# Optimization experiments

Measured on AMD Instinct MI355X. Metric: run time of the kernel, lower is better.

The kernel has to match this reference:

```python
import jax, jax.numpy as jnp
import numpy as np

B = 16
DRUG_LEN, PROT_LEN = 64, 1200
DIM, CONV = 64, 40


def conv1d(x, w, b):
    # x: [B, C_in, L], w: [C_out, C_in, K] (torch layout), VALID padding
    y = jax.lax.conv_general_dilated(
        x, w, window_strides=(1,), padding='VALID',
        dimension_numbers=('NCH', 'OIH', 'NCH'))
    return y + b[None, :, None]


def setup_inputs() -> dict:
    key = jax.random.key(0)
    ks = jax.random.split(key, 32)
    s = 0.05
    inp = {
        'drug_tokens': jax.random.randint(ks[0], (B, DRUG_LEN), 0, 65, dtype=jnp.int32),
        'protein_tokens': jax.random.randint(ks[1], (B, PROT_LEN), 0, 26, dtype=jnp.int32),
        'drug_emb': (jax.random.normal(ks[2], (65, DIM)) * s).at[0].set(0.0),
        'prot_emb': (jax.random.normal(ks[3], (26, DIM)) * s).at[0].set(0.0),
        'dW1': jax.random.normal(ks[4], (CONV, DIM, 4)) * s,
        'db1': jax.random.normal(ks[5], (CONV,)) * s,
        'dW2': jax.random.normal(ks[6], (CONV * 2, CONV, 6)) * s,
        'db2': jax.random.normal(ks[7], (CONV * 2,)) * s,
        'dW3': jax.random.normal(ks[8], (CONV * 4, CONV * 2, 8)) * s,
        'db3': jax.random.normal(ks[9], (CONV * 4,)) * s,
        'pW1': jax.random.normal(ks[10], (CONV, DIM, 4)) * s,
        'pb1': jax.random.normal(ks[11], (CONV,)) * s,
        'pW2': jax.random.normal(ks[12], (CONV * 2, CONV, 8)) * s,
        'pb2': jax.random.normal(ks[13], (CONV * 2,)) * s,
        'pW3': jax.random.normal(ks[14], (CONV * 4, CONV * 2, 12)) * s,
        'pb3': jax.random.normal(ks[15], (CONV * 4,)) * s,
        'dattW': jax.random.normal(ks[16], (160, 160)) * s,
        'dattb': jax.random.normal(ks[17], (160,)) * s,
        'pattW': jax.random.normal(ks[18], (160, 160)) * s,
        'pattb': jax.random.normal(ks[19], (160,)) * s,
        'attW': jax.random.normal(ks[20], (160, 160)) * s,
        'attb': jax.random.normal(ks[21], (160,)) * s,
        'fc1W': jax.random.normal(ks[22], (1024, 320)) * s,
        'fc1b': jax.random.normal(ks[23], (1024,)) * s,
        'fc2W': jax.random.normal(ks[24], (1024, 1024)) * s,
        'fc2b': jax.random.normal(ks[25], (1024,)) * s,
        'fc3W': jax.random.normal(ks[26], (512, 1024)) * s,
        'fc3b': jax.random.normal(ks[27], (512,)) * s,
        'outW': jax.random.normal(ks[28], (2, 512)) * s,
        'outb': jax.random.normal(ks[29], (2,)) * s,
    }
    return inp


def reference(drug_tokens, protein_tokens, drug_emb, prot_emb,
              dW1, db1, dW2, db2, dW3, db3,
              pW1, pb1, pW2, pb2, pW3, pb3,
              dattW, dattb, pattW, pattb, attW, attb,
              fc1W, fc1b, fc2W, fc2b, fc3W, fc3b, outW, outb):
    relu = jax.nn.relu
    # Embedding lookup, then to [B, C, L]
    de = drug_emb[drug_tokens].transpose(0, 2, 1)    # [B,64,64]
    pe = prot_emb[protein_tokens].transpose(0, 2, 1)  # [B,64,1200]
    # CNN stacks
    dc = relu(conv1d(relu(conv1d(relu(conv1d(de, dW1, db1)), dW2, db2)), dW3, db3))  # [B,160,49]
    pc = relu(conv1d(relu(conv1d(relu(conv1d(pe, pW1, pb1)), pW2, pb2)), pW3, pb3))  # [B,160,1179]
    # Per-token attention projections (Linear over channel dim)
    d_att = jnp.einsum('bcd,oc->bdo', dc, dattW) + dattb   # [B,49,160]
    p_att = jnp.einsum('bcp,oc->bpo', pc, pattW) + pattb   # [B,1179,160]
    # Broadcast outer-sum + ReLU + Linear  -> [B,49,1179,160]
    A = relu(d_att[:, :, None, :] + p_att[:, None, :, :])
    A = jnp.einsum('bdpk,ok->bdpo', A, attW) + attb
    comp_atte = jax.nn.sigmoid(jnp.mean(A, axis=2)).transpose(0, 2, 1)  # [B,160,49]
    prot_atte = jax.nn.sigmoid(jnp.mean(A, axis=1)).transpose(0, 2, 1)  # [B,160,1179]
    dc = dc * 0.5 + dc * comp_atte
    pc = pc * 0.5 + pc * prot_atte
    # Global max pool over length
    dvec = jnp.max(dc, axis=2)  # [B,160]
    pvec = jnp.max(pc, axis=2)  # [B,160]
    pair = jnp.concatenate([dvec, pvec], axis=1)  # [B,320]
    # MLP head (dropout = identity at inference)
    h = jax.nn.leaky_relu(pair @ fc1W.T + fc1b, 0.01)
    h = jax.nn.leaky_relu(h @ fc2W.T + fc2b, 0.01)
    h = jax.nn.leaky_relu(h @ fc3W.T + fc3b, 0.01)
    return h @ outW.T + outb  # [B,2]
```

## Files before the change

kernel.cpp:

```cpp
#include <hip/hip_runtime.h>
#include <hip/hip_bf16.h>

typedef __hip_bfloat16 bf16;
typedef __attribute__((ext_vector_type(8))) short short8;
typedef __attribute__((ext_vector_type(4))) float floatx4;

#define NB 16


__device__ __forceinline__ float b2f(bf16 x) { return __bfloat162float(x); }
__device__ __forceinline__ float u16bf(unsigned short u) {
    return __uint_as_float(((unsigned)u) << 16);
}
__device__ __forceinline__ unsigned short f2bu(float v) {
    union { bf16 h; unsigned short u; } cv;
    cv.h = __float2bfloat16(v);
    return cv.u;
}

__global__ void sniff_kernel(const unsigned short* __restrict__ w, int* __restrict__ flag) {
    __shared__ int cnt;
    if (threadIdx.x == 0) cnt = 0;
    __syncthreads();
    int hits = 0;
    for (int s = 0; s < 4; s++) {
        unsigned short u = w[(threadIdx.x * 4 + s) * 2];
        float v = fabsf(u16bf(u));
        if (v > 1e-6f && v < 2.0f) hits++;
    }
    atomicAdd(&cnt, hits);
    __syncthreads();
    if (threadIdx.x == 0) *flag = (cnt > 512) ? 1 : 0;
}

#define NSEG 14
struct CvtJob {
    const void* src[NSEG];
    float* dst[NSEG];
    int n[NSEG];
};
#define NPK 11
struct PackJob {
    const void* src[NPK];
    bf16* dst[NPK];
    short Cout[NPK], CIN[NPK], K[NPK], coP[NPK], CIP[NPK];
};

__global__ void prep(CvtJob cj, PackJob pj, const int* __restrict__ flagp) {
    int y = blockIdx.y;
    int i = blockIdx.x * 256 + threadIdx.x;
    if (y < NSEG) {
        if (i >= cj.n[y]) return;
        const void* s = cj.src[y];
        if (s == nullptr) { cj.dst[y][i] = 0.f; return; }
        cj.dst[y][i] = (*flagp) ? b2f(((const bf16*)s)[i]) : ((const float*)s)[i];
    } else {
        int p = y - NSEG;
        int Cout = pj.Cout[p], CIN = pj.CIN[p], K = pj.K[p];
        int coP = pj.coP[p], CIP = pj.CIP[p];
        int total = K * coP * CIP;
        if (i >= total) return;
        int ci = i % CIP;
        int t = i / CIP;
        int co = t % coP;
        int k = t / coP;
        float v = 0.f;
        if (co < Cout && ci < CIN) {
            int s = (co * CIN + ci) * K + k;
            v = (*flagp) ? b2f(((const bf16*)pj.src[p])[s]) : ((const float*)pj.src[p])[s];
        }
        pj.dst[p][i] = __float2bfloat16(v);
    }
}

template <int K, int CIN, int CHUNKS, int NW>
__device__ __forceinline__ void conv_body(unsigned short* xT,
                                          const unsigned short* xb,
                                          const unsigned short* wbase,
                                          const float* __restrict__ bias,
                                          bf16* __restrict__ y,
                                          int b, int Lin, int Lout,
                                          int Cout, int coP, int l0) {
    const int CIP = CHUNKS * 32;
    const int PCI = CIP + 8;
    const int TLX = 64 + K - 1;
    for (int i = threadIdx.x; i < TLX * CIP; i += NW * 64) {
        int ci = i / TLX, l = i - ci * TLX;
        unsigned short v = 0;
        int gl = l0 + l;
        if (ci < CIN && gl < Lin) v = xb[ci * Lin + gl];
        xT[l * PCI + ci] = v;
    }
    __syncthreads();
    int lane = threadIdx.x & 63;
    int ct = threadIdx.x >> 6;
    int n = lane & 15, quad = lane >> 4;
    floatx4 acc[4];
#pragma unroll
    for (int i = 0; i < 4; i++) acc[i] = (floatx4){0.f, 0.f, 0.f, 0.f};
#pragma unroll
    for (int k = 0; k < K; k++) {
#pragma unroll
        for (int ch = 0; ch < CHUNKS; ch++) {
            short8 a = *(const short8*)(wbase +
                        ((size_t)(k * coP + ct * 16 + n)) * CIP + ch * 32 + quad * 8);
#pragma unroll
            for (int nt = 0; nt < 4; nt++) {
                short8 bb = *(const short8*)(xT + (nt * 16 + n + k) * PCI + ch * 32 + quad * 8);
                acc[nt] = __builtin_amdgcn_mfma_f32_16x16x32_bf16(a, bb, acc[nt], 0, 0, 0);
            }
        }
    }
    int m0 = quad * 4;
#pragma unroll
    for (int nt = 0; nt < 4; nt++) {
        int l = l0 + nt * 16 + n;
        if (l >= Lout) continue;
#pragma unroll
        for (int r = 0; r < 4; r++) {
            int co = ct * 16 + m0 + r;
            if (co < Cout)
                y[((size_t)b * Cout + co) * Lout + l] =
                    __float2bfloat16(fmaxf(acc[nt][r] + bias[co], 0.f));
        }
    }
}

template <int KD, int KP, int CIN, int CHUNKS, int NW>
__global__ __launch_bounds__(NW * 64) void conv_dual(const bf16* __restrict__ xd,
                                                 const bf16* __restrict__ Wpd,
                                                 const float* __restrict__ bd,
                                                 bf16* __restrict__ yd, int LinD, int LoutD,
                                                 const bf16* __restrict__ xp,
                                                 const bf16* __restrict__ Wpp,
                                                 const float* __restrict__ bp,
                                                 bf16* __restrict__ yp, int LinP, int LoutP,
                                                 int Cout, int coP) {
    const int CIP = CHUNKS * 32;
    const int PCI = CIP + 8;
    const int TLXMAX = 64 + KP - 1;
    __shared__ __align__(16) unsigned short xT[TLXMAX * PCI];
    if (blockIdx.x < 16) {
        int b = blockIdx.x;
        conv_body<KD, CIN, CHUNKS, NW>(xT, (const unsigned short*)xd + (size_t)b * CIN * LinD,
                                   (const unsigned short*)Wpd, bd, yd, b, LinD, LoutD,
                                   Cout, coP, 0);
    } else {
        int bx = blockIdx.x - 16;
        int b = bx / 19, l0 = (bx % 19) << 6;
        conv_body<KP, CIN, CHUNKS, NW>(xT, (const unsigned short*)xp + (size_t)b * CIN * LinP,
                                   (const unsigned short*)Wpp, bp, yp, b, LinP, LoutP,
                                   Cout, coP, l0);
    }
}

template <int K, int CIN, int CHUNKS, int NW>
__device__ __forceinline__ void conv_proj_phase(unsigned short* xT, unsigned short* xP,
                                                const unsigned short* xb,
                                                const unsigned short* wbase,
                                                const float* __restrict__ bias,
                                                unsigned short* __restrict__ y,
                                                int b, int Lin, int Lout,
                                                int Cout, int coP, int l0) {
    const int CIP = CHUNKS * 32;
    const int PCI = CIP + 8;
    const int TLX = 64 + K - 1;
    for (int i = threadIdx.x; i < TLX * CIP; i += NW * 64) {
        int ci = i / TLX, l = i - ci * TLX;
        unsigned short v = 0;
        int gl = l0 + l;
        if (ci < CIN && gl < Lin) v = xb[ci * Lin + gl];
        xT[l * PCI + ci] = v;
    }
    __syncthreads();
    int lane = threadIdx.x & 63;
    int ct = threadIdx.x >> 6;
    int n = lane & 15, quad = lane >> 4;
    floatx4 acc[4];
#pragma unroll
    for (int i = 0; i < 4; i++) acc[i] = (floatx4){0.f, 0.f, 0.f, 0.f};
#pragma unroll
    for (int k = 0; k < K; k++) {
#pragma unroll
        for (int ch = 0; ch < CHUNKS; ch++) {
            short8 a = *(const short8*)(wbase +
                        ((size_t)(k * coP + ct * 16 + n)) * CIP + ch * 32 + quad * 8);
#pragma unroll
            for (int nt = 0; nt < 4; nt++) {
                short8 bb = *(const short8*)(xT + (nt * 16 + n + k) * PCI + ch * 32 + quad * 8);
                acc[nt] = __builtin_amdgcn_mfma_f32_16x16x32_bf16(a, bb, acc[nt], 0, 0, 0);
            }
        }
    }
    int m0 = quad * 4;
#pragma unroll
    for (int nt = 0; nt < 4; nt++) {
        int ll = nt * 16 + n;
        int l = l0 + ll;
#pragma unroll
        for (int r = 0; r < 4; r++) {
            int co = ct * 16 + m0 + r;
            float val = (l < Lout) ? fmaxf(acc[nt][r] + bias[co], 0.f) : 0.f;
            unsigned short u = f2bu(val);
            xP[ll * 168 + co] = u;
            if (l < Lout) y[((size_t)b * Cout + co) * Lout + l] = u;
        }
    }
}

template <int KD, int KP, int CIN, int CHUNKS, int NW>
__global__ __launch_bounds__(NW * 64) void conv3_proj(
        const bf16* __restrict__ xd, const bf16* __restrict__ Wpd,
        const float* __restrict__ bd, bf16* __restrict__ yd, int LinD, int LoutD,
        const bf16* __restrict__ xp, const bf16* __restrict__ Wpp,
        const float* __restrict__ bp, bf16* __restrict__ yp, int LinP, int LoutP,
        int Cout, int coP,
        const bf16* __restrict__ dWB, const bf16* __restrict__ pWB,
        const float* __restrict__ dbF, const float* __restrict__ pbF,
        float* __restrict__ datt, bf16* __restrict__ pattB) {
    const int CIP = CHUNKS * 32;
    const int PCI = CIP + 8;
    const int TLXMAX = 64 + KP - 1;
    __shared__ __align__(16) unsigned short xT[TLXMAX * PCI];
    __shared__ __align__(16) unsigned short xP[64 * 168];
    bool isD = blockIdx.x < 16;
    int b, l0, L;
    if (isD) {
        b = blockIdx.x; l0 = 0; L = LoutD;
        conv_proj_phase<KD, CIN, CHUNKS, NW>(xT, xP,
            (const unsigned short*)xd + (size_t)b * CIN * LinD,
            (const unsigned short*)Wpd, bd, (unsigned short*)yd, b, LinD, LoutD, Cout, coP, 0);
    } else {
        int bx = blockIdx.x - 16;
        b = bx / 19; l0 = (bx % 19) << 6; L = LoutP;
        conv_proj_phase<KP, CIN, CHUNKS, NW>(xT, xP,
            (const unsigned short*)xp + (size_t)b * CIN * LinP,
            (const unsigned short*)Wpp, bp, (unsigned short*)yp, b, LinP, LoutP, Cout, coP, l0);
    }
    __syncthreads();
    int lane = threadIdx.x & 63;
    int t = threadIdx.x >> 6;
    int n = lane & 15, quad = lane >> 4;
    const unsigned short* W = (const unsigned short*)(isD ? dWB : pWB);
    const float* pbias = isD ? dbF : pbF;
    floatx4 acc[4];
#pragma unroll
    for (int i = 0; i < 4; i++) acc[i] = (floatx4){0.f, 0.f, 0.f, 0.f};
#pragma unroll
    for (int ch = 0; ch < 5; ch++) {
        short8 a = *(const short8*)(W + ((size_t)(t * 16 + n)) * 160 + ch * 32 + quad * 8);
#pragma unroll
        for (int nt = 0; nt < 4; nt++) {
            short8 bb = *(const short8*)(xP + (nt * 16 + n) * 168 + ch * 32 + quad * 8);
            acc[nt] = __builtin_amdgcn_mfma_f32_16x16x32_bf16(a, bb, acc[nt], 0, 0, 0);
        }
    }
    int m0 = quad * 4;
    int o0 = t * 16 + m0;
#pragma unroll
    for (int nt = 0; nt < 4; nt++) {
        int l = l0 + nt * 16 + n;
        if (l >= L) continue;
        if (isD) {
            float4 v;
            v.x = acc[nt][0] + pbias[o0 + 0];
            v.y = acc[nt][1] + pbias[o0 + 1];
            v.z = acc[nt][2] + pbias[o0 + 2];
            v.w = acc[nt][3] + pbias[o0 + 3];
            *(float4*)(datt + ((size_t)b * 49 + l) * 160 + o0) = v;
        } else {
            ushort4 u;
            u.x = f2bu(acc[nt][0] + pbias[o0 + 0]);
            u.y = f2bu(acc[nt][1] + pbias[o0 + 1]);
            u.z = f2bu(acc[nt][2] + pbias[o0 + 2]);
            u.w = f2bu(acc[nt][3] + pbias[o0 + 3]);
            *(ushort4*)((unsigned short*)pattB + ((size_t)b * 1179 + l) * 160 + o0) = u;
        }
    }
}

__global__ __launch_bounds__(256) void conv1_mfma(const int* __restrict__ dtok,
                                                  const int* __restrict__ ptok,
                                                  const bf16* __restrict__ embDB,
                                                  const bf16* __restrict__ embPB,
                                                  const bf16* __restrict__ dW1p,
                                                  const bf16* __restrict__ pW1p,
                                                  const float* __restrict__ db1f,
                                                  const float* __restrict__ pb1f,
                                                  bf16* __restrict__ d1,
                                                  bf16* __restrict__ p1) {
    const int K = 4, CIP = 64, PCI = 72, TLX = 67, coP = 48, Cout = 40;
    __shared__ __align__(16) unsigned short xT[TLX * PCI];
    __shared__ int stok[TLX];
    bool isD = blockIdx.x < 16;
    int b, l0, Lin, Lout;
    const int* tok; const unsigned short* embB; const unsigned short* Wp;
    const float* bias; bf16* y;
    if (isD) {
        b = blockIdx.x; l0 = 0; Lin = 64; Lout = 61;
        tok = dtok; embB = (const unsigned short*)embDB;
        Wp = (const unsigned short*)dW1p; bias = db1f; y = d1;
    } else {
        int bx = blockIdx.x - 16;
        b = bx / 19; l0 = (bx % 19) << 6; Lin = 1200; Lout = 1197;
        tok = ptok; embB = (const unsigned short*)embPB;
        Wp = (const unsigned short*)pW1p; bias = pb1f; y = p1;
    }
    if (threadIdx.x < TLX) {
        int l = l0 + threadIdx.x;
        stok[threadIdx.x] = (l < Lin) ? tok[b * Lin + l] : -1;
    }
    __syncthreads();
    for (int i = threadIdx.x; i < TLX * CIP; i += 256) {
        int ci = i / TLX, l = i - ci * TLX;
        int t = stok[l];
        xT[l * PCI + ci] = (t >= 0) ? embB[t * 64 + ci] : (unsigned short)0;
    }
    __syncthreads();
    int lane = threadIdx.x & 63;
    int w = threadIdx.x >> 6;
    int n = lane & 15, quad = lane >> 4;
    if (w >= 3) return;
    floatx4 acc[4];
#pragma unroll
    for (int i = 0; i < 4; i++) acc[i] = (floatx4){0.f, 0.f, 0.f, 0.f};
#pragma unroll
    for (int k = 0; k < K; k++) {
#pragma unroll
        for (int ch = 0; ch < 2; ch++) {
            short8 a = *(const short8*)(Wp +
                        ((size_t)(k * coP + w * 16 + n)) * CIP + ch * 32 + quad * 8);
#pragma unroll
            for (int nt = 0; nt < 4; nt++) {
                short8 bb = *(const short8*)(xT + (nt * 16 + n + k) * PCI + ch * 32 + quad * 8);
                acc[nt] = __builtin_amdgcn_mfma_f32_16x16x32_bf16(a, bb, acc[nt], 0, 0, 0);
            }
        }
    }
    int m0 = quad * 4;
#pragma unroll
    for (int nt = 0; nt < 4; nt++) {
        int l = l0 + nt * 16 + n;
        if (l >= Lout) continue;
#pragma unroll
        for (int r = 0; r < 4; r++) {
            int co = w * 16 + m0 + r;
            if (co < Cout)
                y[((size_t)b * Cout + co) * Lout + l] =
                    __float2bfloat16(fmaxf(acc[nt][r] + bias[co], 0.f));
        }
    }
}

__global__ __launch_bounds__(640) void mean_fused(const float* __restrict__ datt,
                                                  const bf16* __restrict__ patt,
                                                  bf16* __restrict__ MpW,
                                                  float* __restrict__ Mdpart) {
    __shared__ __align__(16) unsigned short sp[37 * 160];
    int tid = threadIdx.x;
    int b = blockIdx.x >> 5;
    int pc = blockIdx.x & 31;
    int p0 = pc * 37;
    int pmax = 1179 - p0;
    if (pmax > 37) pmax = 37;
    {
        const short8* src = (const short8*)((const unsigned short*)patt +
                                            ((size_t)b * 1179 + p0) * 160);
        short8* dst = (short8*)sp;
        int n8 = (pmax * 160) >> 3;
        for (int v = tid; v < n8; v += 640) dst[v] = src[v];
    }
    int h = tid & 3;
    int k = tid >> 2;
    int d0 = h * 13;
    int nd = (h == 3) ? 10 : 13;
    const float* drow = datt + (size_t)b * 49 * 160 + k;
    float dv[13], md[13];
#pragma unroll
    for (int i = 0; i < 13; i++) {
        dv[i] = (i < nd) ? drow[(d0 + i) * 160] : -1e30f;
        md[i] = 0.f;
    }
    __syncthreads();
    unsigned short* mp = (unsigned short*)MpW + ((size_t)b * 1184 + p0) * 160 + k;
#pragma unroll 2
    for (int pi = 0; pi < pmax; pi++) {
        float pv = u16bf(sp[pi * 160 + k]);
        float s0 = 0.f, s1 = 0.f, s2 = 0.f, s3 = 0.f;
#pragma unroll
        for (int g = 0; g < 3; g++) {
            float r0 = fmaxf(dv[g * 4 + 0] + pv, 0.f);
            float r1 = fmaxf(dv[g * 4 + 1] + pv, 0.f);
            float r2 = fmaxf(dv[g * 4 + 2] + pv, 0.f);
            float r3 = fmaxf(dv[g * 4 + 3] + pv, 0.f);
            md[g * 4 + 0] += r0; s0 += r0;
            md[g * 4 + 1] += r1; s1 += r1;
            md[g * 4 + 2] += r2; s2 += r2;
            md[g * 4 + 3] += r3; s3 += r3;
        }
        {
            float r = fmaxf(dv[12] + pv, 0.f);
            md[12] += r; s0 += r;
        }
        float s = (s0 + s1) + (s2 + s3);
        s += __shfl_xor(s, 1, 64);
        s += __shfl_xor(s, 2, 64);
        if (h == 0) mp[(size_t)pi * 160] = f2bu(s * (1.f / 49.f));
    }
    float* op = Mdpart + (((size_t)b * 32 + pc) * 49) * 160 + k;
#pragma unroll
    for (int i = 0; i < 13; i++)
        if (i < nd) op[(d0 + i) * 160] = md[i];
}

__global__ __launch_bounds__(640) void att_sig_mfma(const float* __restrict__ Mdpart,
                                                    const bf16* __restrict__ MpW,
                                                    const bf16* __restrict__ wattB,
                                                    const float* __restrict__ attbF,
                                                    const bf16* __restrict__ dcB,
                                                    const bf16* __restrict__ pcB,
                                                    float* __restrict__ pair) {
    const int PCI = 168;
    __shared__ __align__(16) unsigned short sM[64 * PCI];
    bool isD = blockIdx.x < 16;
    int b, p0, L, off;
    const unsigned short* conv;
    if (isD) {
        b = blockIdx.x; p0 = 0; L = 49; off = 0; conv = (const unsigned short*)dcB;
        const float* mdp = Mdpart + (size_t)b * 32 * 49 * 160;
        for (int i = threadIdx.x; i < 160 * 64; i += 640) {
            int r = i / 160, k = i - r * 160;
            float v = 0.f;
            if (r < 49) {
                const float* src = mdp + r * 160 + k;
                float s0 = 0.f, s1 = 0.f, s2 = 0.f, s3 = 0.f;
#pragma unroll
                for (int pc = 0; pc < 32; pc += 4) {
                    s0 += src[(size_t)(pc + 0) * 7840];
                    s1 += src[(size_t)(pc + 1) * 7840];
                    s2 += src[(size_t)(pc + 2) * 7840];
                    s3 += src[(size_t)(pc + 3) * 7840];
                }
                v = ((s0 + s1) + (s2 + s3)) * (1.f / 1179.f);
            }
            sM[r * PCI + k] = f2bu(v);
        }
    } else {
        int bx = blockIdx.x - 16;
        b = bx / 19; p0 = (bx % 19) << 6; L = 1179; off = 160;
        conv = (const unsigned short*)pcB;
        const unsigned short* mb = (const unsigned short*)MpW + (size_t)b * 1184 * 160;
        for (int i = threadIdx.x; i < 160 * 64; i += 640) {
            int r = i / 160, k = i - r * 160;
            int p = p0 + r;
            sM[r * PCI + k] = (p < 1179) ? mb[(size_t)p * 160 + k] : (unsigned short)0;
        }
    }
    __syncthreads();
    int lane = threadIdx.x & 63;
    int t = threadIdx.x >> 6;
    int n = lane & 15, quad = lane >> 4;
    floatx4 acc[4];
#pragma unroll
    for (int i = 0; i < 4; i++) acc[i] = (floatx4){0.f, 0.f, 0.f, 0.f};
    const unsigned short* W = (const unsigned short*)wattB;
#pragma unroll
    for (int ch = 0; ch < 5; ch++) {
        short8 a = *(const short8*)(W + ((size_t)(t * 16 + n)) * 160 + ch * 32 + quad * 8);
#pragma unroll
        for (int nt = 0; nt < 4; nt++) {
            short8 bb = *(const short8*)(sM + (nt * 16 + n) * PCI + ch * 32 + quad * 8);
            acc[nt] = __builtin_amdgcn_mfma_f32_16x16x32_bf16(a, bb, acc[nt], 0, 0, 0);
        }
    }
    int m0 = quad * 4;
    float vmax[4] = {0.f, 0.f, 0.f, 0.f};
#pragma unroll
    for (int nt = 0; nt < 4; nt++) {
        int p = p0 + nt * 16 + n;
#pragma unroll
        for (int r = 0; r < 4; r++) {
            int o = t * 16 + m0 + r;
            float sig = 1.f / (1.f + __expf(-(acc[nt][r] + attbF[o])));
            float v = 0.f;
            if (p < L) v = u16bf(conv[((size_t)b * 160 + o) * L + p]) * (0.5f + sig);
            vmax[r] = fmaxf(vmax[r], v);
        }
    }
#pragma unroll
    for (int m = 1; m < 16; m <<= 1) {
#pragma unroll
        for (int r = 0; r < 4; r++)
            vmax[r] = fmaxf(vmax[r], __shfl_xor(vmax[r], m, 64));
    }
    if (n == 0) {
#pragma unroll
        for (int r = 0; r < 4; r++)
            atomicMax((unsigned int*)(pair + b * 320 + off + t * 16 + m0 + r),
                      __float_as_uint(vmax[r]));
    }
}

__global__ __launch_bounds__(256) void fc_block(const float* __restrict__ in,
                                                const void* __restrict__ W,
                                                const float* __restrict__ bias,
                                                float* __restrict__ out,
                                                int IN, int OUT,
                                                const int* __restrict__ flagp) {
    int j = blockIdx.x;
    int w = threadIdx.x >> 6, li = threadIdx.x & 63;
    int nv = IN >> 2;
    const float4* i0 = (const float4*)(in + (size_t)(w * 4 + 0) * IN);
    const float4* i1 = (const float4*)(in + (size_t)(w * 4 + 1) * IN);
    const float4* i2 = (const float4*)(in + (size_t)(w * 4 + 2) * IN);
    const float4* i3 = (const float4*)(in + (size_t)(w * 4 + 3) * IN);
    float p0 = 0.f, p1 = 0.f, p2 = 0.f, p3 = 0.f;
    if (*flagp) {
        const ushort4* w4 = (const ushort4*)((const unsigned short*)W + (size_t)j * IN);
        for (int v = li; v < nv; v += 64) {
            ushort4 u = w4[v];
            float wa = u16bf(u.x), wb = u16bf(u.y), wc = u16bf(u.z), wd = u16bf(u.w);
            float4 x;
            x = i0[v]; p0 += x.x * wa + x.y * wb + x.z * wc + x.w * wd;
            x = i1[v]; p1 += x.x * wa + x.y * wb + x.z * wc + x.w * wd;
            x = i2[v]; p2 += x.x * wa + x.y * wb + x.z * wc + x.w * wd;
            x = i3[v]; p3 += x.x * wa + x.y * wb + x.z * wc + x.w * wd;
        }
    } else {
        const float4* w4 = (const float4*)((const float*)W + (size_t)j * IN);
        for (int v = li; v < nv; v += 64) {
            float4 u = w4[v];
            float4 x;
            x = i0[v]; p0 += x.x * u.x + x.y * u.y + x.z * u.z + x.w * u.w;
            x = i1[v]; p1 += x.x * u.x + x.y * u.y + x.z * u.z + x.w * u.w;
            x = i2[v]; p2 += x.x * u.x + x.y * u.y + x.z * u.z + x.w * u.w;
            x = i3[v]; p3 += x.x * u.x + x.y * u.y + x.z * u.z + x.w * u.w;
        }
    }
#pragma unroll
    for (int m = 1; m < 64; m <<= 1) {
        p0 += __shfl_xor(p0, m, 64);
        p1 += __shfl_xor(p1, m, 64);
        p2 += __shfl_xor(p2, m, 64);
        p3 += __shfl_xor(p3, m, 64);
    }
    if (li == 0) {
        float bj = bias[j];
        float o0 = p0 + bj, o1 = p1 + bj, o2 = p2 + bj, o3 = p3 + bj;
        o0 = o0 > 0.f ? o0 : 0.01f * o0;
        o1 = o1 > 0.f ? o1 : 0.01f * o1;
        o2 = o2 > 0.f ? o2 : 0.01f * o2;
        o3 = o3 > 0.f ? o3 : 0.01f * o3;
        out[(size_t)(w * 4 + 0) * OUT + j] = o0;
        out[(size_t)(w * 4 + 1) * OUT + j] = o1;
        out[(size_t)(w * 4 + 2) * OUT + j] = o2;
        out[(size_t)(w * 4 + 3) * OUT + j] = o3;
    }
}

__global__ __launch_bounds__(256) void out_block(const float* __restrict__ h,
                                                 const void* __restrict__ W,
                                                 const float* __restrict__ biasF,
                                                 void* __restrict__ out,
                                                 const int* __restrict__ flagp) {
    int j = blockIdx.x;
    int w = threadIdx.x >> 6, li = threadIdx.x & 63;
    const int IN = 512, nv = 128;
    const float4* i0 = (const float4*)(h + (size_t)(w * 4 + 0) * IN);
    const float4* i1 = (const float4*)(h + (size_t)(w * 4 + 1) * IN);
    const float4* i2 = (const float4*)(h + (size_t)(w * 4 + 2) * IN);
    const float4* i3 = (const float4*)(h + (size_t)(w * 4 + 3) * IN);
    float p0 = 0.f, p1 = 0.f, p2 = 0.f, p3 = 0.f;
    int flag = *flagp;
    if (flag) {
        const ushort4* w4 = (const ushort4*)((const unsigned short*)W + (size_t)j * IN);
        for (int v = li; v < nv; v += 64) {
            ushort4 u = w4[v];
            float wa = u16bf(u.x), wb = u16bf(u.y), wc = u16bf(u.z), wd = u16bf(u.w);
            float4 x;
            x = i0[v]; p0 += x.x * wa + x.y * wb + x.z * wc + x.w * wd;
            x = i1[v]; p1 += x.x * wa + x.y * wb + x.z * wc + x.w * wd;
            x = i2[v]; p2 += x.x * wa + x.y * wb + x.z * wc + x.w * wd;
            x = i3[v]; p3 += x.x * wa + x.y * wb + x.z * wc + x.w * wd;
        }
    } else {
        const float4* w4 = (const float4*)((const float*)W + (size_t)j * IN);
        for (int v = li; v < nv; v += 64) {
            float4 u = w4[v];
            float4 x;
            x = i0[v]; p0 += x.x * u.x + x.y * u.y + x.z * u.z + x.w * u.w;
            x = i1[v]; p1 += x.x * u.x + x.y * u.y + x.z * u.z + x.w * u.w;
            x = i2[v]; p2 += x.x * u.x + x.y * u.y + x.z * u.z + x.w * u.w;
            x = i3[v]; p3 += x.x * u.x + x.y * u.y + x.z * u.z + x.w * u.w;
        }
    }
#pragma unroll
    for (int m = 1; m < 64; m <<= 1) {
        p0 += __shfl_xor(p0, m, 64);
        p1 += __shfl_xor(p1, m, 64);
        p2 += __shfl_xor(p2, m, 64);
        p3 += __shfl_xor(p3, m, 64);
    }
    if (li == 0) {
        float bj = biasF[j];
        float o0 = p0 + bj, o1 = p1 + bj, o2 = p2 + bj, o3 = p3 + bj;
        if (flag) {
            bf16* ob = (bf16*)out;
            ob[(w * 4 + 0) * 2 + j] = __float2bfloat16(o0);
            ob[(w * 4 + 1) * 2 + j] = __float2bfloat16(o1);
            ob[(w * 4 + 2) * 2 + j] = __float2bfloat16(o2);
            ob[(w * 4 + 3) * 2 + j] = __float2bfloat16(o3);
        } else {
            float* of = (float*)out;
            of[(w * 4 + 0) * 2 + j] = o0;
            of[(w * 4 + 1) * 2 + j] = o1;
            of[(w * 4 + 2) * 2 + j] = o2;
            of[(w * 4 + 3) * 2 + j] = o3;
        }
    }
}

extern "C" void kernel_launch(void* const* d_in, const int* in_sizes, int n_in,
                              void* d_out, int out_size, void* d_ws, size_t ws_size,
                              hipStream_t stream) {
    const int* drug_tok = (const int*)d_in[0];
    const int* prot_tok = (const int*)d_in[1];
    const void* drug_emb = d_in[2];
    const void* prot_emb = d_in[3];
    const void* dW1 = d_in[4];  const void* db1 = d_in[5];
    const void* dW2 = d_in[6];  const void* db2 = d_in[7];
    const void* dW3 = d_in[8];  const void* db3 = d_in[9];
    const void* pW1 = d_in[10]; const void* pb1 = d_in[11];
    const void* pW2 = d_in[12]; const void* pb2 = d_in[13];
    const void* pW3 = d_in[14]; const void* pb3 = d_in[15];
    const void* dattW = d_in[16]; const void* dattb = d_in[17];
    const void* pattW = d_in[18]; const void* pattb = d_in[19];
    const void* attW  = d_in[20]; const void* attb  = d_in[21];
    const void* fc1W = d_in[22]; const void* fc1b = d_in[23];
    const void* fc2W = d_in[24]; const void* fc2b = d_in[25];
    const void* fc3W = d_in[26]; const void* fc3b = d_in[27];
    const void* outW = d_in[28]; const void* outb = d_in[29];

    char* base = (char*)d_ws;
    size_t cur = 0;
    auto alloc = [&](size_t bytes) -> char* {
        char* p = base + cur;
        cur = (cur + bytes + 255) & ~(size_t)255;
        return p;
    };
    int*   flag  = (int*)alloc(256);
    bf16* embDB = (bf16*)alloc(65 * 64 * 2);
    bf16* embPB = (bf16*)alloc(26 * 64 * 2);
    bf16* dW1p = (bf16*)alloc((size_t)4 * 48 * 64 * 2);
    bf16* pW1p = (bf16*)alloc((size_t)4 * 48 * 64 * 2);
    bf16* dW2p = (bf16*)alloc((size_t)6 * 128 * 64 * 2);
    bf16* dW3p = (bf16*)alloc((size_t)8 * 192 * 96 * 2);
    bf16* pW2p = (bf16*)alloc((size_t)8 * 128 * 64 * 2);
    bf16* pW3p = (bf16*)alloc((size_t)12 * 192 * 96 * 2);
    float* db1f = (float*)alloc(40 * 4);
    float* db2f = (float*)alloc(80 * 4);
    float* db3f = (float*)alloc(160 * 4);
    float* pb1f = (float*)alloc(40 * 4);
    float* pb2f = (float*)alloc(80 * 4);
    float* pb3f = (float*)alloc(160 * 4);
    float* dattbF = (float*)alloc(160 * 4);
    float* pattbF = (float*)alloc(160 * 4);
    float* attbF  = (float*)alloc(160 * 4);
    float* fc1bF = (float*)alloc(1024 * 4);
    float* fc2bF = (float*)alloc(1024 * 4);
    float* fc3bF = (float*)alloc(512 * 4);
    float* outbF = (float*)alloc(2 * 4);
    bf16* dattWB = (bf16*)alloc(25600 * 2);
    bf16* pattWB = (bf16*)alloc(25600 * 2);
    bf16* wattB  = (bf16*)alloc(25600 * 2);
    bf16* d1  = (bf16*)alloc((size_t)NB * 40 * 61 * 2);
    bf16* d2  = (bf16*)alloc((size_t)NB * 80 * 56 * 2);
    bf16* dcB = (bf16*)alloc((size_t)NB * 160 * 49 * 2);
    bf16* p1  = (bf16*)alloc((size_t)NB * 40 * 1197 * 2);
    bf16* p2  = (bf16*)alloc((size_t)NB * 80 * 1190 * 2);
    bf16* pcB = (bf16*)alloc((size_t)NB * 160 * 1179 * 2);
    float* datt  = (float*)alloc((size_t)NB * 49 * 160 * 4);
    bf16* pattB = (bf16*)alloc((size_t)NB * 1179 * 160 * 2);
    float* Mdpart = (float*)alloc((size_t)NB * 32 * 49 * 160 * 4);
    bf16* MpW  = (bf16*)alloc((size_t)NB * 1184 * 160 * 2);
    float* pair = (float*)alloc(NB * 320 * 4);
    float* h1 = (float*)alloc(NB * 1024 * 4);
    float* h2 = (float*)alloc(NB * 1024 * 4);
    float* h3 = (float*)alloc(NB * 512 * 4);

    sniff_kernel<<<1, 256, 0, stream>>>((const unsigned short*)fc2W, flag);

    CvtJob cj;
    int si = 0;
    auto add = [&](const void* s, float* d, int n) { cj.src[si] = s; cj.dst[si] = d; cj.n[si] = n; si++; };
    add(db1, db1f, 40); add(db2, db2f, 80); add(db3, db3f, 160);
    add(pb1, pb1f, 40); add(pb2, pb2f, 80); add(pb3, pb3f, 160);
    add(dattb, dattbF, 160); add(pattb, pattbF, 160); add(attb, attbF, 160);
    add(fc1b, fc1bF, 1024); add(fc2b, fc2bF, 1024); add(fc3b, fc3bF, 512);
    add(outb, outbF, 2);
    add(nullptr, pair, NB * 320);
    PackJob pj;
    int pi = 0;
    auto seg = [&](const void* s, bf16* d, int Cout, int CIN, int K, int coP, int CIP) {
        pj.src[pi] = s; pj.dst[pi] = d;
        pj.Cout[pi] = Cout; pj.CIN[pi] = CIN; pj.K[pi] = K; pj.coP[pi] = coP; pj.CIP[pi] = CIP;
        pi++;
    };
    seg(dW1, dW1p, 40, 64, 4, 48, 64);
    seg(pW1, pW1p, 40, 64, 4, 48, 64);
    seg(dW2, dW2p, 80, 40, 6, 128, 64);
    seg(pW2, pW2p, 80, 40, 8, 128, 64);
    seg(dW3, dW3p, 160, 80, 8, 192, 96);
    seg(pW3, pW3p, 160, 80, 12, 192, 96);
    seg(dattW, dattWB, 160, 160, 1, 160, 160);
    seg(pattW, pattWB, 160, 160, 1, 160, 160);
    seg(attW,  wattB,  160, 160, 1, 160, 160);
    seg(drug_emb, embDB, 65, 64, 1, 65, 64);
    seg(prot_emb, embPB, 26, 64, 1, 26, 64);
    prep<<<dim3(864, NSEG + NPK), 256, 0, stream>>>(cj, pj, flag);

    conv1_mfma<<<16 + 16 * 19, 256, 0, stream>>>(drug_tok, prot_tok, embDB, embPB,
                                                 dW1p, pW1p, db1f, pb1f, d1, p1);
    conv_dual<6, 8, 40, 2, 5><<<320, 320, 0, stream>>>(
        d1, dW2p, db2f, d2, 61, 56,
        p1, pW2p, pb2f, p2, 1197, 1190, 80, 128);
    conv3_proj<8, 12, 80, 3, 10><<<320, 640, 0, stream>>>(
        d2, dW3p, db3f, dcB, 56, 49,
        p2, pW3p, pb3f, pcB, 1190, 1179, 160, 192,
        dattWB, pattWB, dattbF, pattbF, datt, pattB);

    mean_fused<<<16 * 32, 640, 0, stream>>>(datt, pattB, MpW, Mdpart);

    att_sig_mfma<<<320, 640, 0, stream>>>(Mdpart, MpW, wattB, attbF, dcB, pcB, pair);

    fc_block<<<1024, 256, 0, stream>>>(pair, fc1W, fc1bF, h1, 320, 1024, flag);
    fc_block<<<1024, 256, 0, stream>>>(h1, fc2W, fc2bF, h2, 1024, 1024, flag);
    fc_block<<<512, 256, 0, stream>>>(h2, fc3W, fc3bF, h3, 1024, 512, flag);
    out_block<<<2, 256, 0, stream>>>(h3, outW, outbF, d_out, flag);
}
```

Measured before the change: 241.8 us.

## Vectorize conv input staging, pad conv1 output stride, flatten prep launch grid

```diff
diff --git a/kernel.cpp b/kernel.cpp
--- a/kernel.cpp
+++ b/kernel.cpp
@@ -37,7 +37,6 @@
 struct CvtJob {
     const void* src[NSEG];
     float* dst[NSEG];
-    int n[NSEG];
 };
 #define NPK 11
 struct PackJob {
@@ -45,29 +44,33 @@
     bf16* dst[NPK];
     short Cout[NPK], CIN[NPK], K[NPK], coP[NPK], CIP[NPK];
 };
-
-__global__ void prep(CvtJob cj, PackJob pj, const int* __restrict__ flagp) {
-    int y = blockIdx.y;
-    int i = blockIdx.x * 256 + threadIdx.x;
-    if (y < NSEG) {
-        if (i >= cj.n[y]) return;
-        const void* s = cj.src[y];
-        if (s == nullptr) { cj.dst[y][i] = 0.f; return; }
-        cj.dst[y][i] = (*flagp) ? b2f(((const bf16*)s)[i]) : ((const float*)s)[i];
+struct PrepOff { int off[NSEG + NPK + 1]; };
+
+__global__ void prep(CvtJob cj, PackJob pj, PrepOff po, const int* __restrict__ flagp) {
+    int g = blockIdx.x * 256 + threadIdx.x;
+    if (g >= po.off[NSEG + NPK]) return;
+    int s = 0;
+#pragma unroll
+    for (int t = 1; t < NSEG + NPK; t++)
+        if (g >= po.off[t]) s = t;
+    int i = g - po.off[s];
+    if (s < NSEG) {
+        const void* sp = cj.src[s];
+        if (sp == nullptr) { cj.dst[s][i] = 0.f; return; }
+        cj.dst[s][i] = (*flagp) ? b2f(((const bf16*)sp)[i]) : ((const float*)sp)[i];
     } else {
-        int p = y - NSEG;
+        int p = s - NSEG;
         int Cout = pj.Cout[p], CIN = pj.CIN[p], K = pj.K[p];
         int coP = pj.coP[p], CIP = pj.CIP[p];
-        int total = K * coP * CIP;
-        if (i >= total) return;
+        (void)K;
         int ci = i % CIP;
         int t = i / CIP;
         int co = t % coP;
         int k = t / coP;
         float v = 0.f;
         if (co < Cout && ci < CIN) {
-            int s = (co * CIN + ci) * K + k;
-            v = (*flagp) ? b2f(((const bf16*)pj.src[p])[s]) : ((const float*)pj.src[p])[s];
+            int si = (co * CIN + ci) * pj.K[p] + k;
+            v = (*flagp) ? b2f(((const bf16*)pj.src[p])[si]) : ((const float*)pj.src[p])[si];
         }
         pj.dst[p][i] = __float2bfloat16(v);
     }
@@ -79,17 +82,27 @@
                                           const unsigned short* wbase,
                                           const float* __restrict__ bias,
                                           bf16* __restrict__ y,
-                                          int b, int Lin, int Lout,
+                                          int b, int Lin, int Lstride, int Lout,
                                           int Cout, int coP, int l0) {
     const int CIP = CHUNKS * 32;
     const int PCI = CIP + 8;
     const int TLX = 64 + K - 1;
-    for (int i = threadIdx.x; i < TLX * CIP; i += NW * 64) {
-        int ci = i / TLX, l = i - ci * TLX;
-        unsigned short v = 0;
-        int gl = l0 + l;
-        if (ci < CIN && gl < Lin) v = xb[ci * Lin + gl];
-        xT[l * PCI + ci] = v;
+    const int LV = (TLX + 7) >> 3;
+    for (int i = threadIdx.x; i < CIP * LV; i += NW * 64) {
+        int ci = i / LV, lv = (i - ci * LV) << 3;
+        if (ci < CIN && lv + 8 <= TLX && l0 + lv + 8 <= Lin) {
+            short8 v = *(const short8*)(xb + ci * Lstride + l0 + lv);
+#pragma unroll
+            for (int j = 0; j < 8; j++) xT[(lv + j) * PCI + ci] = (unsigned short)v[j];
+        } else {
+            for (int j = 0; j < 8; j++) {
+                int l = lv + j;
+                if (l >= TLX) break;
+                int gl = l0 + l;
+                xT[l * PCI + ci] = (ci < CIN && gl < Lin) ? xb[ci * Lstride + gl]
+                                                          : (unsigned short)0;
+            }
+        }
     }
     __syncthreads();
     int lane = threadIdx.x & 63;
@@ -130,11 +143,13 @@
 __global__ __launch_bounds__(NW * 64) void conv_dual(const bf16* __restrict__ xd,
                                                  const bf16* __restrict__ Wpd,
                                                  const float* __restrict__ bd,
-                                                 bf16* __restrict__ yd, int LinD, int LoutD,
+                                                 bf16* __restrict__ yd,
+                                                 int LinD, int LsD, int LoutD,
                                                  const bf16* __restrict__ xp,
                                                  const bf16* __restrict__ Wpp,
                                                  const float* __restrict__ bp,
-                                                 bf16* __restrict__ yp, int LinP, int LoutP,
+                                                 bf16* __restrict__ yp,
+                                                 int LinP, int LsP, int LoutP,
                                                  int Cout, int coP) {
     const int CIP = CHUNKS * 32;
     const int PCI = CIP + 8;
@@ -142,14 +157,14 @@
     __shared__ __align__(16) unsigned short xT[TLXMAX * PCI];
     if (blockIdx.x < 16) {
         int b = blockIdx.x;
-        conv_body<KD, CIN, CHUNKS, NW>(xT, (const unsigned short*)xd + (size_t)b * CIN * LinD,
-                                   (const unsigned short*)Wpd, bd, yd, b, LinD, LoutD,
+        conv_body<KD, CIN, CHUNKS, NW>(xT, (const unsigned short*)xd + (size_t)b * CIN * LsD,
+                                   (const unsigned short*)Wpd, bd, yd, b, LinD, LsD, LoutD,
                                    Cout, coP, 0);
     } else {
         int bx = blockIdx.x - 16;
         int b = bx / 19, l0 = (bx % 19) << 6;
-        conv_body<KP, CIN, CHUNKS, NW>(xT, (const unsigned short*)xp + (size_t)b * CIN * LinP,
-                                   (const unsigned short*)Wpp, bp, yp, b, LinP, LoutP,
+        conv_body<KP, CIN, CHUNKS, NW>(xT, (const unsigned short*)xp + (size_t)b * CIN * LsP,
+                                   (const unsigned short*)Wpp, bp, yp, b, LinP, LsP, LoutP,
                                    Cout, coP, l0);
     }
 }
@@ -165,12 +180,22 @@
     const int CIP = CHUNKS * 32;
     const int PCI = CIP + 8;
     const int TLX = 64 + K - 1;
-    for (int i = threadIdx.x; i < TLX * CIP; i += NW * 64) {
-        int ci = i / TLX, l = i - ci * TLX;
-        unsigned short v = 0;
-        int gl = l0 + l;
-        if (ci < CIN && gl < Lin) v = xb[ci * Lin + gl];
-        xT[l * PCI + ci] = v;
+    const int LV = (TLX + 7) >> 3;
+    for (int i = threadIdx.x; i < CIP * LV; i += NW * 64) {
+        int ci = i / LV, lv = (i - ci * LV) << 3;
+        if (ci < CIN && lv + 8 <= TLX && l0 + lv + 8 <= Lin) {
+            short8 v = *(const short8*)(xb + ci * Lin + l0 + lv);
+#pragma unroll
+            for (int j = 0; j < 8; j++) xT[(lv + j) * PCI + ci] = (unsigned short)v[j];
+        } else {
+            for (int j = 0; j < 8; j++) {
+                int l = lv + j;
+                if (l >= TLX) break;
+                int gl = l0 + l;
+                xT[l * PCI + ci] = (ci < CIN && gl < Lin) ? xb[ci * Lin + gl]
+                                                          : (unsigned short)0;
+            }
+        }
     }
     __syncthreads();
     int lane = threadIdx.x & 63;
@@ -293,16 +318,16 @@
     __shared__ __align__(16) unsigned short xT[TLX * PCI];
     __shared__ int stok[TLX];
     bool isD = blockIdx.x < 16;
-    int b, l0, Lin, Lout;
+    int b, l0, Lin, Lout, Ostride;
     const int* tok; const unsigned short* embB; const unsigned short* Wp;
     const float* bias; bf16* y;
     if (isD) {
-        b = blockIdx.x; l0 = 0; Lin = 64; Lout = 61;
+        b = blockIdx.x; l0 = 0; Lin = 64; Lout = 61; Ostride = 62;
         tok = dtok; embB = (const unsigned short*)embDB;
         Wp = (const unsigned short*)dW1p; bias = db1f; y = d1;
     } else {
         int bx = blockIdx.x - 16;
-        b = bx / 19; l0 = (bx % 19) << 6; Lin = 1200; Lout = 1197;
+        b = bx / 19; l0 = (bx % 19) << 6; Lin = 1200; Lout = 1197; Ostride = 1198;
         tok = ptok; embB = (const unsigned short*)embPB;
         Wp = (const unsigned short*)pW1p; bias = pb1f; y = p1;
     }
@@ -311,10 +336,12 @@
         stok[threadIdx.x] = (l < Lin) ? tok[b * Lin + l] : -1;
     }
     __syncthreads();
-    for (int i = threadIdx.x; i < TLX * CIP; i += 256) {
-        int ci = i / TLX, l = i - ci * TLX;
+    for (int i = threadIdx.x; i < TLX * 8; i += 256) {
+        int l = i >> 3, c8 = (i & 7) << 3;
         int t = stok[l];
-        xT[l * PCI + ci] = (t >= 0) ? embB[t * 64 + ci] : (unsigned short)0;
+        short8 v = (short8){0, 0, 0, 0, 0, 0, 0, 0};
+        if (t >= 0) v = *(const short8*)(embB + t * 64 + c8);
+        *(short8*)(xT + l * PCI + c8) = v;
     }
     __syncthreads();
     int lane = threadIdx.x & 63;
@@ -346,7 +373,7 @@
         for (int r = 0; r < 4; r++) {
             int co = w * 16 + m0 + r;
             if (co < Cout)
-                y[((size_t)b * Cout + co) * Lout + l] =
+                y[((size_t)b * Cout + co) * Ostride + l] =
                     __float2bfloat16(fmaxf(acc[nt][r] + bias[co], 0.f));
         }
     }
@@ -673,10 +700,10 @@
     bf16* dattWB = (bf16*)alloc(25600 * 2);
     bf16* pattWB = (bf16*)alloc(25600 * 2);
     bf16* wattB  = (bf16*)alloc(25600 * 2);
-    bf16* d1  = (bf16*)alloc((size_t)NB * 40 * 61 * 2);
+    bf16* d1  = (bf16*)alloc((size_t)NB * 40 * 62 * 2);
     bf16* d2  = (bf16*)alloc((size_t)NB * 80 * 56 * 2);
     bf16* dcB = (bf16*)alloc((size_t)NB * 160 * 49 * 2);
-    bf16* p1  = (bf16*)alloc((size_t)NB * 40 * 1197 * 2);
+    bf16* p1  = (bf16*)alloc((size_t)NB * 40 * 1198 * 2);
     bf16* p2  = (bf16*)alloc((size_t)NB * 80 * 1190 * 2);
     bf16* pcB = (bf16*)alloc((size_t)NB * 160 * 1179 * 2);
     float* datt  = (float*)alloc((size_t)NB * 49 * 160 * 4);
@@ -691,20 +718,23 @@
     sniff_kernel<<<1, 256, 0, stream>>>((const unsigned short*)fc2W, flag);
 
     CvtJob cj;
-    int si = 0;
-    auto add = [&](const void* s, float* d, int n) { cj.src[si] = s; cj.dst[si] = d; cj.n[si] = n; si++; };
+    PackJob pj;
+    PrepOff po;
+    int si = 0, running = 0;
+    auto add = [&](const void* s, float* d, int n) {
+        cj.src[si] = s; cj.dst[si] = d; po.off[si] = running; running += n; si++;
+    };
     add(db1, db1f, 40); add(db2, db2f, 80); add(db3, db3f, 160);
     add(pb1, pb1f, 40); add(pb2, pb2f, 80); add(pb3, pb3f, 160);
     add(dattb, dattbF, 160); add(pattb, pattbF, 160); add(attb, attbF, 160);
     add(fc1b, fc1bF, 1024); add(fc2b, fc2bF, 1024); add(fc3b, fc3bF, 512);
     add(outb, outbF, 2);
     add(nullptr, pair, NB * 320);
-    PackJob pj;
     int pi = 0;
     auto seg = [&](const void* s, bf16* d, int Cout, int CIN, int K, int coP, int CIP) {
         pj.src[pi] = s; pj.dst[pi] = d;
         pj.Cout[pi] = Cout; pj.CIN[pi] = CIN; pj.K[pi] = K; pj.coP[pi] = coP; pj.CIP[pi] = CIP;
-        pi++;
+        po.off[NSEG + pi] = running; running += K * coP * CIP; pi++;
     };
     seg(dW1, dW1p, 40, 64, 4, 48, 64);
     seg(pW1, pW1p, 40, 64, 4, 48, 64);
@@ -717,13 +747,14 @@
     seg(attW,  wattB,  160, 160, 1, 160, 160);
     seg(drug_emb, embDB, 65, 64, 1, 65, 64);
     seg(prot_emb, embPB, 26, 64, 1, 26, 64);
-    prep<<<dim3(864, NSEG + NPK), 256, 0, stream>>>(cj, pj, flag);
+    po.off[NSEG + NPK] = running;
+    prep<<<(running + 255) / 256, 256, 0, stream>>>(cj, pj, po, flag);
 
     conv1_mfma<<<16 + 16 * 19, 256, 0, stream>>>(drug_tok, prot_tok, embDB, embPB,
                                                  dW1p, pW1p, db1f, pb1f, d1, p1);
     conv_dual<6, 8, 40, 2, 5><<<320, 320, 0, stream>>>(
-        d1, dW2p, db2f, d2, 61, 56,
-        p1, pW2p, pb2f, p2, 1197, 1190, 80, 128);
+        d1, dW2p, db2f, d2, 61, 62, 56,
+        p1, pW2p, pb2f, p2, 1197, 1198, 1190, 80, 128);
     conv3_proj<8, 12, 80, 3, 10><<<320, 640, 0, stream>>>(
         d2, dW3p, db3f, dcB, 56, 49,
         p2, pW3p, pb3f, pcB, 1190, 1179, 160, 192,
```

After: 238.9 us. Within noise of the previous version (-1.2%).
